# Optimization experiments

Hardware: AMD Instinct MI355X
Metric: run time of the kernel (lower is better)

Reference implementation:

```python
import jax, jax.numpy as jnp
import numpy as np

N_NODES = 20000


def _segment_softmax(alpha, dst, num_nodes):
    # numerically-stable softmax over edges grouped by destination node
    m = jax.ops.segment_max(alpha, dst, num_segments=num_nodes)
    m = jnp.where(jnp.isfinite(m), m, 0.0)
    a = jnp.exp(alpha - m[dst])
    denom = jax.ops.segment_sum(a, dst, num_segments=num_nodes)
    return a / denom[dst]


def mgcn_conv(x, src, dst, edge_type, basis, att, weight, root, bias, num_nodes):
    # x: [N, in], basis: [B, in, out], att: [R, B], weight: [R, out=in]
    x_i = x[dst]                                   # [E, in] target feats
    x_j = x[src]                                   # [E, in] source feats
    # per-edge attention logit: sum_d x_i[d] * w_r[d] * x_j[d]
    alpha = jnp.sum(x_i * weight[edge_type] * x_j, axis=1)   # [E]
    alpha = _segment_softmax(alpha, dst, num_nodes)          # [E]
    # basis-decomposed per-edge transform: x_j @ (att_r . basis)
    t = jnp.einsum('ei,bio->ebo', x_j, basis)                # [E, B, out]
    msg = jnp.einsum('ebo,eb->eo', t, att[edge_type])        # [E, out]
    msg = msg * alpha[:, None]
    out = jax.ops.segment_sum(msg, dst, num_segments=num_nodes)  # [N, out]
    return out + x @ root + bias


def setup_inputs() -> dict:
    key = jax.random.key(0)
    ks = jax.random.split(key, 16)
    E, D, R, B, N = 32768, 128, 474, 64, N_NODES
    s = 0.05
    return {
        'entity': jnp.arange(N, dtype=jnp.int64) if jax.config.jax_enable_x64 else jnp.arange(N, dtype=jnp.int32),
        'edge_index': jax.random.randint(ks[0], (2, E), 0, N, dtype=jnp.int32),
        'edge_type': jax.random.randint(ks[1], (E,), 0, R, dtype=jnp.int32),
        'emb_table': jax.random.normal(ks[2], (N, D), dtype=jnp.float32),
        'basis1': jax.random.normal(ks[3], (B, D, D), dtype=jnp.float32) * s,
        'att1': jax.random.normal(ks[4], (R, B), dtype=jnp.float32) * s,
        'weight1': jax.random.normal(ks[5], (R, D), dtype=jnp.float32) * s,
        'root1': jax.random.normal(ks[6], (D, D), dtype=jnp.float32) * s,
        'bias1': jnp.zeros((D,), dtype=jnp.float32),
        'basis2': jax.random.normal(ks[7], (B, D, D), dtype=jnp.float32) * s,
        'att2': jax.random.normal(ks[8], (R, B), dtype=jnp.float32) * s,
        'weight2': jax.random.normal(ks[9], (R, D), dtype=jnp.float32) * s,
        'root2': jax.random.normal(ks[10], (D, D), dtype=jnp.float32) * s,
        'bias2': jnp.zeros((D,), dtype=jnp.float32),
    }


def reference(entity, edge_index, edge_type, emb_table,
              basis1, att1, weight1, root1, bias1,
              basis2, att2, weight2, root2, bias2):
    src, dst = edge_index[0], edge_index[1]   # PyG: (source j, target i)
    x = emb_table[entity]                     # embedding lookup
    h = jax.nn.relu(mgcn_conv(x, src, dst, edge_type, basis1, att1,
                              weight1, root1, bias1, N_NODES))
    # dropout is identity at inference
    out = mgcn_conv(h, src, dst, edge_type, basis2, att2,
                    weight2, root2, bias2, N_NODES)
    return out
```

## Files before the change

### kernel.cpp

```cpp
#include <hip/hip_runtime.h>
#include <hip/hip_bf16.h>

#define N_NODES 20000
#define N_EDGES 32768
#define DIM 128
#define N_REL 474
#define N_BASIS 64
#define TILE_E 64
#define MAXCH (N_EDGES / TILE_E + N_REL)
#define WSTRIDE 260

typedef __bf16 bf16x8 __attribute__((ext_vector_type(8)));
typedef float f32x4 __attribute__((ext_vector_type(4)));

__device__ __forceinline__ unsigned short f2b(float f) {
    unsigned u = __float_as_uint(f);
    unsigned r = (u + 0x7FFFu + ((u >> 16) & 1u)) >> 16;
    return (unsigned short)r;
}
__device__ __forceinline__ float b2f(unsigned short s) {
    return __uint_as_float(((unsigned)s) << 16);
}
__device__ __forceinline__ __bf16 u2b(unsigned short u) {
    union { unsigned short u; __bf16 b; } c; c.u = u; return c.b;
}

__global__ __launch_bounds__(256) void prep_kernel(const float4* __restrict__ emb,
                                                   const int* __restrict__ entity,
                                                   const int* __restrict__ etype,
                                                   ushort4* __restrict__ xb4,
                                                   float4* __restrict__ zreg, int zcount4,
                                                   int* __restrict__ cnt) {
    int gtid = blockIdx.x * 256 + threadIdx.x;
    int gsz = gridDim.x * 256;
    int total4 = N_NODES * DIM / 4;
    for (int i = gtid; i < total4; i += gsz) {
        int n = i >> 5, rem = i & 31;
        float4 v = emb[(size_t)entity[n] * 32 + rem];
        ushort4 s;
        s.x = f2b(v.x); s.y = f2b(v.y); s.z = f2b(v.z); s.w = f2b(v.w);
        xb4[i] = s;
    }
    for (int e = gtid; e < N_EDGES; e += gsz) atomicAdd(&cnt[etype[e]], 1);
    float4 z = make_float4(0.f, 0.f, 0.f, 0.f);
    for (int i = gtid; i < zcount4; i += gsz) zreg[i] = z;
}

__global__ void scanr_kernel(const int* __restrict__ cnt, int* __restrict__ offs,
                             int* __restrict__ cursor, int* __restrict__ chunk_r,
                             int* __restrict__ chunk_o, int* __restrict__ nchunks,
                             int R, int E) {
    __shared__ int s[512];
    int t = threadIdx.x;
    int v = (t < R) ? cnt[t] : 0;
    s[t] = v;
    __syncthreads();
    for (int d = 1; d < 512; d <<= 1) {
        int add = (t >= d) ? s[t - d] : 0;
        __syncthreads();
        s[t] += add;
        __syncthreads();
    }
    int excl = s[t] - v;
    if (t < R) { offs[t] = excl; cursor[t] = excl; }
    if (t == 0) offs[R] = E;
    int nc = (v + TILE_E - 1) / TILE_E;
    if (t < R && nc > 0) {
        int b = atomicAdd(nchunks, nc);
        for (int c = 0; c < nc; c++) { chunk_r[b + c] = t; chunk_o[b + c] = excl + c * TILE_E; }
    }
}

__global__ void scatter_kernel(const int* __restrict__ et, int* __restrict__ cursor,
                               int* __restrict__ eids, int E) {
    int e = blockIdx.x * blockDim.x + threadIdx.x;
    if (e < E) {
        int p = atomicAdd(&cursor[et[e]], 1);
        eids[p] = e;
    }
}

__global__ __launch_bounds__(256) void logitexp_kernel(const unsigned short* __restrict__ xb,
                                                       const float* __restrict__ w,
                                                       const int* __restrict__ src,
                                                       const int* __restrict__ dst,
                                                       const int* __restrict__ et,
                                                       float* __restrict__ alpha,
                                                       float* __restrict__ den, int E) {
    int wid = (blockIdx.x * 256 + threadIdx.x) >> 6;
    int lane = threadIdx.x & 63;
    if (wid >= E) return;
    int s = src[wid], d = dst[wid], r = et[wid];
    unsigned ax = ((const unsigned*)(xb + (size_t)s * DIM))[lane];
    unsigned bx = ((const unsigned*)(xb + (size_t)d * DIM))[lane];
    float2 wv = ((const float2*)(w + (size_t)r * DIM))[lane];
    float v = b2f((unsigned short)(ax & 0xFFFF)) * wv.x * b2f((unsigned short)(bx & 0xFFFF))
            + b2f((unsigned short)(ax >> 16)) * wv.y * b2f((unsigned short)(bx >> 16));
    for (int off = 32; off > 0; off >>= 1) v += __shfl_xor(v, off, 64);
    if (lane == 0) {
        float a = expf(v);
        alpha[wid] = a;
        atomicAdd(&den[d], a);
    }
}

__global__ __launch_bounds__(256) void wmix_kernel(const float* __restrict__ att,
                                                   const float* __restrict__ basis,
                                                   unsigned short* __restrict__ W, int R) {
    int io0 = blockIdx.x * 256;
    int r0 = blockIdx.y * 64;
    __shared__ unsigned short bt[64 * WSTRIDE];
    int t = threadIdx.x;
#pragma unroll
    for (int p = 0; p < 16; p++) {
        int c = t + 256 * p;
        int k = c >> 6, of = c & 63;
        float4 v = *(const float4*)(basis + (size_t)k * (DIM * DIM) + io0 + of * 4);
        ushort4 s;
        s.x = f2b(v.x); s.y = f2b(v.y); s.z = f2b(v.z); s.w = f2b(v.w);
        *(ushort4*)&bt[k * WSTRIDE + of * 4] = s;
    }
    __syncthreads();

    int w = t >> 6, l = t & 63, n = l & 15, q = l >> 4;
    f32x4 acc[4][4] = {};
#pragma unroll
    for (int kb = 0; kb < 2; kb++) {
        int kbase = kb * 32 + q * 8;
        bf16x8 a[4];
#pragma unroll
        for (int rt = 0; rt < 4; rt++) {
            int rm = min(r0 + rt * 16 + n, R - 1);
            const float* ap = att + (size_t)rm * N_BASIS + kbase;
#pragma unroll
            for (int j = 0; j < 8; j++) a[rt][j] = u2b(f2b(ap[j]));
        }
#pragma unroll
        for (int c = 0; c < 4; c++) {
            int ob = w * 64 + c * 16 + n;
            bf16x8 b;
#pragma unroll
            for (int j = 0; j < 8; j++) b[j] = u2b(bt[(kbase + j) * WSTRIDE + ob]);
#pragma unroll
            for (int rt = 0; rt < 4; rt++)
                acc[rt][c] = __builtin_amdgcn_mfma_f32_16x16x32_bf16(a[rt], b, acc[rt][c], 0, 0, 0);
        }
    }
#pragma unroll
    for (int rt = 0; rt < 4; rt++) {
#pragma unroll
        for (int c = 0; c < 4; c++) {
            int col = io0 + w * 64 + c * 16 + n;
#pragma unroll
            for (int rg = 0; rg < 4; rg++) {
                int r = r0 + rt * 16 + q * 4 + rg;
                if (r < R) W[(size_t)r * (DIM * DIM) + col] = f2b(acc[rt][c][rg]);
            }
        }
    }
}

__global__ __launch_bounds__(256) void msg_kernel(const unsigned short* __restrict__ xb,
                                                  const unsigned short* __restrict__ W,
                                                  const int* __restrict__ chunk_r,
                                                  const int* __restrict__ chunk_off,
                                                  const int* __restrict__ nchunks,
                                                  const int* __restrict__ eids,
                                                  const int* __restrict__ offs,
                                                  const int* __restrict__ src,
                                                  const int* __restrict__ dst,
                                                  const float* __restrict__ ae,
                                                  const float* __restrict__ denom,
                                                  float* __restrict__ outacc) {
    if ((int)blockIdx.x >= *nchunks) return;
    int r = chunk_r[blockIdx.x];
    int base = chunk_off[blockIdx.x];
    int nE = min(TILE_E, offs[r + 1] - base);
    const unsigned short* Wr = W + (size_t)r * (DIM * DIM);

    __shared__ unsigned short wt[128 * 136];
    __shared__ unsigned short xjf[8192];
    __shared__ float scf[TILE_E];
    __shared__ int sdd[TILE_E];

    int t = threadIdx.x;
    if (t < TILE_E) {
        if (t < nE) {
            int e = eids[base + t];
            int d_ = dst[e];
            sdd[t] = d_;
            scf[t] = ae[e] / denom[d_];
        } else { sdd[t] = 0; scf[t] = 0.f; }
    }
#pragma unroll
    for (int p = 0; p < 4; p++) {
        int c = t + 256 * p;
        int g = c >> 6;
        int rt = g >> 2, kb = g & 3;
        int q = (c >> 4) & 3, m = c & 15;
        int e = rt * 16 + m;
        int oct = kb * 4 + q;
        int4 v = make_int4(0, 0, 0, 0);
        if (e < nE)
            v = *(const int4*)(xb + (size_t)src[eids[base + e]] * DIM + oct * 8);
        *(int4*)&xjf[c * 8] = v;
    }
#pragma unroll
    for (int p = 0; p < 8; p++) {
        int c = t + 256 * p;
        int k = c >> 4, oct = c & 15;
        int4 v = *(const int4*)(Wr + k * DIM + oct * 8);
        *(int4*)&wt[k * 136 + oct * 8] = v;
    }
    __syncthreads();

    int w = t >> 6, l = t & 63, n = l & 15, q = l >> 4;
    f32x4 acc[2][4] = {};
#pragma unroll
    for (int kb = 0; kb < 4; kb++) {
        bf16x8 a[4];
#pragma unroll
        for (int rt = 0; rt < 4; rt++) a[rt] = *(const bf16x8*)&xjf[((rt * 4 + kb) * 64 + l) * 8];
        int kbase = kb * 32 + q * 8;
#pragma unroll
        for (int c = 0; c < 2; c++) {
            int ob = (w * 2 + c) * 16 + n;
            bf16x8 b;
#pragma unroll
            for (int j = 0; j < 8; j++) b[j] = u2b(wt[(kbase + j) * 136 + ob]);
#pragma unroll
            for (int rt = 0; rt < 4; rt++)
                acc[c][rt] = __builtin_amdgcn_mfma_f32_16x16x32_bf16(a[rt], b, acc[c][rt], 0, 0, 0);
        }
    }
#pragma unroll
    for (int c = 0; c < 2; c++) {
        int col = (w * 2 + c) * 16 + n;
#pragma unroll
        for (int rt = 0; rt < 4; rt++) {
#pragma unroll
            for (int rg = 0; rg < 4; rg++) {
                int e = rt * 16 + q * 4 + rg;
                if (e < nE)
                    atomicAdd(&outacc[(size_t)sdd[e] * DIM + col], scf[e] * acc[c][rt][rg]);
            }
        }
    }
}

__global__ __launch_bounds__(256) void root_kernel(const unsigned short* __restrict__ xb,
                                                   const float* __restrict__ rootM,
                                                   const float* __restrict__ bias,
                                                   const float* __restrict__ accbuf,
                                                   unsigned short* __restrict__ outb,
                                                   float* __restrict__ outf,
                                                   int mode, int N) {
    int n0 = blockIdx.x * 64;
    __shared__ unsigned short wt[128 * 136];
    __shared__ unsigned short xrf[8192];
    int t = threadIdx.x;
#pragma unroll
    for (int p = 0; p < 4; p++) {
        int c = t + 256 * p;
        int g = c >> 6;
        int rt = g >> 2, kb = g & 3;
        int q = (c >> 4) & 3, m = c & 15;
        int row = n0 + rt * 16 + m;
        int oct = kb * 4 + q;
        int4 v = make_int4(0, 0, 0, 0);
        if (row < N) v = *(const int4*)(xb + (size_t)row * DIM + oct * 8);
        *(int4*)&xrf[c * 8] = v;
    }
#pragma unroll
    for (int p = 0; p < 16; p++) {
        int c = t + 256 * p;
        int k = c >> 5, of = c & 31;
        float4 v = *(const float4*)(rootM + k * DIM + of * 4);
        ushort4 s;
        s.x = f2b(v.x); s.y = f2b(v.y); s.z = f2b(v.z); s.w = f2b(v.w);
        *(ushort4*)&wt[k * 136 + of * 4] = s;
    }
    __syncthreads();

    int w = t >> 6, l = t & 63, n = l & 15, q = l >> 4;
    f32x4 acc[2][4] = {};
#pragma unroll
    for (int kb = 0; kb < 4; kb++) {
        bf16x8 a[4];
#pragma unroll
        for (int rt = 0; rt < 4; rt++) a[rt] = *(const bf16x8*)&xrf[((rt * 4 + kb) * 64 + l) * 8];
        int kbase = kb * 32 + q * 8;
#pragma unroll
        for (int c = 0; c < 2; c++) {
            int ob = (w * 2 + c) * 16 + n;
            bf16x8 b;
#pragma unroll
            for (int j = 0; j < 8; j++) b[j] = u2b(wt[(kbase + j) * 136 + ob]);
#pragma unroll
            for (int rt = 0; rt < 4; rt++)
                acc[c][rt] = __builtin_amdgcn_mfma_f32_16x16x32_bf16(a[rt], b, acc[c][rt], 0, 0, 0);
        }
    }
#pragma unroll
    for (int c = 0; c < 2; c++) {
        int col = (w * 2 + c) * 16 + n;
        float bo = bias[col];
#pragma unroll
        for (int rt = 0; rt < 4; rt++) {
#pragma unroll
            for (int rg = 0; rg < 4; rg++) {
                int row = n0 + rt * 16 + q * 4 + rg;
                if (row < N) {
                    float v = accbuf[(size_t)row * DIM + col] + acc[c][rt][rg] + bo;
                    if (mode) {
                        outb[(size_t)row * DIM + col] = f2b(fmaxf(v, 0.f));
                    } else {
                        outf[(size_t)row * DIM + col] = v;
                    }
                }
            }
        }
    }
}

extern "C" void kernel_launch(void* const* d_in, const int* in_sizes, int n_in,
                              void* d_out, int out_size, void* d_ws, size_t ws_size,
                              hipStream_t stream) {
    const int N = N_NODES, E = N_EDGES, R = N_REL;

    const int* entity = (const int*)d_in[0];
    const int* eidx   = (const int*)d_in[1];
    const int* src    = eidx;
    const int* dst    = eidx + E;
    const int* etype  = (const int*)d_in[2];
    const float* emb  = (const float*)d_in[3];
    const float* basis1 = (const float*)d_in[4];
    const float* att1   = (const float*)d_in[5];
    const float* w1     = (const float*)d_in[6];
    const float* root1  = (const float*)d_in[7];
    const float* bias1  = (const float*)d_in[8];
    const float* basis2 = (const float*)d_in[9];
    const float* att2   = (const float*)d_in[10];
    const float* w2     = (const float*)d_in[11];
    const float* root2  = (const float*)d_in[12];
    const float* bias2  = (const float*)d_in[13];
    float* out = (float*)d_out;

    size_t off = 0;
    auto alloc = [&](size_t bytes) -> void* {
        void* p = (char*)d_ws + off;
        off += (bytes + 255) & ~(size_t)255;
        return p;
    };
    unsigned short* W  = (unsigned short*)alloc((size_t)R * DIM * DIM * 2);
    unsigned short* xb = (unsigned short*)alloc((size_t)N * DIM * 2);
    unsigned short* hb = (unsigned short*)alloc((size_t)N * DIM * 2);
    float* zreg   = (float*)alloc((size_t)(2 * N * DIM + 2 * N) * 4);
    float* acc1   = zreg;
    float* acc2   = zreg + (size_t)N * DIM;
    float* denom1 = zreg + (size_t)2 * N * DIM;
    float* denom2 = denom1 + N;
    float* alpha  = (float*)alloc((size_t)E * 4);
    int* meta     = (int*)alloc((size_t)(R + 1) * 4);
    int* cnt      = meta;
    int* nchunks  = meta + R;
    int* offs     = (int*)alloc((size_t)(R + 1) * 4);
    int* cursor   = (int*)alloc((size_t)R * 4);
    int* eids     = (int*)alloc((size_t)E * 4);
    int* chunk_r  = (int*)alloc((size_t)MAXCH * 4);
    int* chunk_o  = (int*)alloc((size_t)MAXCH * 4);

    int zcount4 = (2 * N * DIM + 2 * N) / 4;

    hipMemsetAsync(meta, 0, (size_t)(R + 1) * 4, stream);
    prep_kernel<<<2048, 256, 0, stream>>>((const float4*)emb, entity, etype,
                                          (ushort4*)xb, (float4*)zreg, zcount4, cnt);
    scanr_kernel<<<1, 512, 0, stream>>>(cnt, offs, cursor, chunk_r, chunk_o, nchunks, R, E);
    scatter_kernel<<<(E + 255) / 256, 256, 0, stream>>>(etype, cursor, eids, E);

    logitexp_kernel<<<E / 4, 256, 0, stream>>>(xb, w1, src, dst, etype, alpha, denom1, E);
    wmix_kernel<<<dim3(64, 8), 256, 0, stream>>>(att1, basis1, W, R);
    msg_kernel<<<MAXCH, 256, 0, stream>>>(xb, W, chunk_r, chunk_o, nchunks,
                                          eids, offs, src, dst, alpha, denom1, acc1);
    root_kernel<<<(N + 63) / 64, 256, 0, stream>>>(xb, root1, bias1, acc1, hb, nullptr, 1, N);

    logitexp_kernel<<<E / 4, 256, 0, stream>>>(hb, w2, src, dst, etype, alpha, denom2, E);
    wmix_kernel<<<dim3(64, 8), 256, 0, stream>>>(att2, basis2, W, R);
    msg_kernel<<<MAXCH, 256, 0, stream>>>(hb, W, chunk_r, chunk_o, nchunks,
                                          eids, offs, src, dst, alpha, denom2, acc2);
    root_kernel<<<(N + 63) / 64, 256, 0, stream>>>(hb, root2, bias2, acc2, nullptr, out, 0, N);
}
```

Before: 247.4 us.

## Fuse edge bucketing into one block kernel and batch both wmix launches

Replaces the histogram-in-prep, scan and scatter kernels plus the memset with a single 512-thread plan kernel. It builds the relation histogram, scan, chunk list and edge permutation in shared memory. Both layers' relation weight mixes now run in one wider launch with separate W buffers, which removes launches and lets the two mixes fill more of the GPU. The trade-off is a serial single-block pass over 32K edges and twice the workspace for W.

```diff
diff --git a/kernel.cpp b/kernel.cpp
--- a/kernel.cpp
+++ b/kernel.cpp
@@ -27,10 +27,8 @@
 
 __global__ __launch_bounds__(256) void prep_kernel(const float4* __restrict__ emb,
                                                    const int* __restrict__ entity,
-                                                   const int* __restrict__ etype,
                                                    ushort4* __restrict__ xb4,
-                                                   float4* __restrict__ zreg, int zcount4,
-                                                   int* __restrict__ cnt) {
+                                                   float4* __restrict__ zreg, int zcount4) {
     int gtid = blockIdx.x * 256 + threadIdx.x;
     int gsz = gridDim.x * 256;
     int total4 = N_NODES * DIM / 4;
@@ -41,41 +39,44 @@
         s.x = f2b(v.x); s.y = f2b(v.y); s.z = f2b(v.z); s.w = f2b(v.w);
         xb4[i] = s;
     }
-    for (int e = gtid; e < N_EDGES; e += gsz) atomicAdd(&cnt[etype[e]], 1);
     float4 z = make_float4(0.f, 0.f, 0.f, 0.f);
     for (int i = gtid; i < zcount4; i += gsz) zreg[i] = z;
 }
 
-__global__ void scanr_kernel(const int* __restrict__ cnt, int* __restrict__ offs,
-                             int* __restrict__ cursor, int* __restrict__ chunk_r,
-                             int* __restrict__ chunk_o, int* __restrict__ nchunks,
-                             int R, int E) {
-    __shared__ int s[512];
+__global__ __launch_bounds__(512) void plan_kernel(const int* __restrict__ etype,
+                                                   int* __restrict__ offs,
+                                                   int* __restrict__ eids,
+                                                   int* __restrict__ chunk_r,
+                                                   int* __restrict__ chunk_o,
+                                                   int* __restrict__ nchunks_g) {
+    __shared__ int hist[512];
+    __shared__ int cur[N_REL];
+    __shared__ int lnc;
     int t = threadIdx.x;
-    int v = (t < R) ? cnt[t] : 0;
-    s[t] = v;
-    __syncthreads();
+    hist[t] = 0;
+    if (t == 0) lnc = 0;
+    __syncthreads();
+    for (int e = t; e < N_EDGES; e += 512) atomicAdd(&hist[etype[e]], 1);
+    __syncthreads();
+    int v = hist[t];
     for (int d = 1; d < 512; d <<= 1) {
-        int add = (t >= d) ? s[t - d] : 0;
+        int add = (t >= d) ? hist[t - d] : 0;
         __syncthreads();
-        s[t] += add;
+        hist[t] += add;
         __syncthreads();
     }
-    int excl = s[t] - v;
-    if (t < R) { offs[t] = excl; cursor[t] = excl; }
-    if (t == 0) offs[R] = E;
-    int nc = (v + TILE_E - 1) / TILE_E;
-    if (t < R && nc > 0) {
-        int b = atomicAdd(nchunks, nc);
-        for (int c = 0; c < nc; c++) { chunk_r[b + c] = t; chunk_o[b + c] = excl + c * TILE_E; }
-    }
-}
-
-__global__ void scatter_kernel(const int* __restrict__ et, int* __restrict__ cursor,
-                               int* __restrict__ eids, int E) {
-    int e = blockIdx.x * blockDim.x + threadIdx.x;
-    if (e < E) {
-        int p = atomicAdd(&cursor[et[e]], 1);
+    int excl = hist[t] - v;
+    if (t < N_REL) { offs[t] = excl; cur[t] = excl; }
+    if (t == 0) offs[N_REL] = N_EDGES;
+    if (t < N_REL && v > 0) {
+        int nc = (v + TILE_E - 1) / TILE_E;
+        int cb = atomicAdd(&lnc, nc);
+        for (int c = 0; c < nc; c++) { chunk_r[cb + c] = t; chunk_o[cb + c] = excl + c * TILE_E; }
+    }
+    __syncthreads();
+    if (t == 0) *nchunks_g = lnc;
+    for (int e = t; e < N_EDGES; e += 512) {
+        int p = atomicAdd(&cur[etype[e]], 1);
         eids[p] = e;
     }
 }
@@ -104,11 +105,17 @@
     }
 }
 
-__global__ __launch_bounds__(256) void wmix_kernel(const float* __restrict__ att,
-                                                   const float* __restrict__ basis,
-                                                   unsigned short* __restrict__ W, int R) {
+__global__ __launch_bounds__(256) void wmix_kernel(const float* __restrict__ att1,
+                                                   const float* __restrict__ basis1,
+                                                   unsigned short* __restrict__ W1,
+                                                   const float* __restrict__ att2,
+                                                   const float* __restrict__ basis2,
+                                                   unsigned short* __restrict__ W2, int R) {
+    const float* att   = (blockIdx.y < 8) ? att1 : att2;
+    const float* basis = (blockIdx.y < 8) ? basis1 : basis2;
+    unsigned short* W  = (blockIdx.y < 8) ? W1 : W2;
     int io0 = blockIdx.x * 256;
-    int r0 = blockIdx.y * 64;
+    int r0 = (blockIdx.y & 7) * 64;
     __shared__ unsigned short bt[64 * WSTRIDE];
     int t = threadIdx.x;
 #pragma unroll
@@ -352,7 +359,8 @@
         off += (bytes + 255) & ~(size_t)255;
         return p;
     };
-    unsigned short* W  = (unsigned short*)alloc((size_t)R * DIM * DIM * 2);
+    unsigned short* W1 = (unsigned short*)alloc((size_t)R * DIM * DIM * 2);
+    unsigned short* W2 = (unsigned short*)alloc((size_t)R * DIM * DIM * 2);
     unsigned short* xb = (unsigned short*)alloc((size_t)N * DIM * 2);
     unsigned short* hb = (unsigned short*)alloc((size_t)N * DIM * 2);
     float* zreg   = (float*)alloc((size_t)(2 * N * DIM + 2 * N) * 4);
@@ -361,32 +369,26 @@
     float* denom1 = zreg + (size_t)2 * N * DIM;
     float* denom2 = denom1 + N;
     float* alpha  = (float*)alloc((size_t)E * 4);
-    int* meta     = (int*)alloc((size_t)(R + 1) * 4);
-    int* cnt      = meta;
-    int* nchunks  = meta + R;
+    int* nchunks  = (int*)alloc(256);
     int* offs     = (int*)alloc((size_t)(R + 1) * 4);
-    int* cursor   = (int*)alloc((size_t)R * 4);
     int* eids     = (int*)alloc((size_t)E * 4);
     int* chunk_r  = (int*)alloc((size_t)MAXCH * 4);
     int* chunk_o  = (int*)alloc((size_t)MAXCH * 4);
 
     int zcount4 = (2 * N * DIM + 2 * N) / 4;
 
-    hipMemsetAsync(meta, 0, (size_t)(R + 1) * 4, stream);
-    prep_kernel<<<2048, 256, 0, stream>>>((const float4*)emb, entity, etype,
-                                          (ushort4*)xb, (float4*)zreg, zcount4, cnt);
-    scanr_kernel<<<1, 512, 0, stream>>>(cnt, offs, cursor, chunk_r, chunk_o, nchunks, R, E);
-    scatter_kernel<<<(E + 255) / 256, 256, 0, stream>>>(etype, cursor, eids, E);
+    prep_kernel<<<2048, 256, 0, stream>>>((const float4*)emb, entity,
+                                          (ushort4*)xb, (float4*)zreg, zcount4);
+    plan_kernel<<<1, 512, 0, stream>>>(etype, offs, eids, chunk_r, chunk_o, nchunks);
+    wmix_kernel<<<dim3(64, 16), 256, 0, stream>>>(att1, basis1, W1, att2, basis2, W2, R);
 
     logitexp_kernel<<<E / 4, 256, 0, stream>>>(xb, w1, src, dst, etype, alpha, denom1, E);
-    wmix_kernel<<<dim3(64, 8), 256, 0, stream>>>(att1, basis1, W, R);
-    msg_kernel<<<MAXCH, 256, 0, stream>>>(xb, W, chunk_r, chunk_o, nchunks,
+    msg_kernel<<<MAXCH, 256, 0, stream>>>(xb, W1, chunk_r, chunk_o, nchunks,
                                           eids, offs, src, dst, alpha, denom1, acc1);
     root_kernel<<<(N + 63) / 64, 256, 0, stream>>>(xb, root1, bias1, acc1, hb, nullptr, 1, N);
 
     logitexp_kernel<<<E / 4, 256, 0, stream>>>(hb, w2, src, dst, etype, alpha, denom2, E);
-    wmix_kernel<<<dim3(64, 8), 256, 0, stream>>>(att2, basis2, W, R);
-    msg_kernel<<<MAXCH, 256, 0, stream>>>(hb, W, chunk_r, chunk_o, nchunks,
+    msg_kernel<<<MAXCH, 256, 0, stream>>>(hb, W2, chunk_r, chunk_o, nchunks,
                                           eids, offs, src, dst, alpha, denom2, acc2);
     root_kernel<<<(N + 63) / 64, 256, 0, stream>>>(hb, root2, bias2, acc2, nullptr, out, 0, N);
 }
```

Measured after the change: 252.3 us. Within noise of the previous version (+2.0%).
